# Kernel tuning notes

Hardware: AMD Instinct MI355X
Metric: run time of the kernel (lower is better)

The kernel has to match this reference:

```python
import jax, jax.numpy as jnp
import numpy as np

VOTE_PERHEAD = 24  # matches init vote_perhead


def setup_inputs() -> dict:
    key = jax.random.key(0)
    kx, = jax.random.split(key, 1)
    B, S, D = 2048, 1024, 12  # batch, seq_len (perfect square 32*32), num_heads channel
    x = jax.random.normal(kx, (B, S, D), dtype=jnp.float32)
    # fixed Gaussian-like smoothing kernel [[1,2,1],[2,4,2],[1,2,1]] (OIHW)
    kernel = jnp.array([[1.0, 2.0, 1.0], [2.0, 4.0, 2.0], [1.0, 2.0, 1.0]],
                       dtype=jnp.float32).reshape(1, 1, 3, 3)
    return {"x": x, "kernel": kernel, "select_num": 24}


def reference(x, kernel, select_num):
    B, S = x.shape[0], x.shape[1]
    # score over non-CLS tokens, channel 0: [B, S-1]
    score = x[:, 1:, 0]
    # top-k vote indices per batch: [B, VOTE_PERHEAD], values in [0, S-2]
    _, select = jax.lax.top_k(score, VOTE_PERHEAD)
    # batched bincount via scatter-add (replaces the per-batch python loop)
    count = jnp.zeros((B, S), dtype=jnp.float32)
    count = count.at[jnp.arange(B)[:, None], select].add(1.0)
    # enhance_local: 2D 3x3 smoothing conv when S is a perfect square
    Hs = int(np.sqrt(S))
    if Hs * Hs == S:
        cnt = count.reshape(B, 1, Hs, Hs)
        cnt = jax.lax.conv_general_dilated(
            cnt, kernel, window_strides=(1, 1), padding=[(1, 1), (1, 1)],
            dimension_numbers=("NCHW", "OIHW", "NCHW"))
        count = cnt.reshape(B, S)
    else:
        k1d = kernel.reshape(1, 1, 9)
        cnt = jax.lax.conv_general_dilated(
            count[:, None, :], k1d, window_strides=(1,), padding=[(4, 4)],
            dimension_numbers=("NCH", "OIH", "NCH"))
        count = cnt.reshape(B, S)
    # descending sort of votes; indices shifted by +1 (skip CLS token)
    patch_idx = jnp.argsort(-count, axis=-1) + 1
    return patch_idx[:, :select_num], count
```

## Files before the change

### kernel.cpp

```cpp
#include <hip/hip_runtime.h>

constexpr int S_ = 1024;
constexpr int D_ = 12;
constexpr int K_ = 24;
constexpr int NT = 256;
constexpr int NL = 5;

__constant__ const unsigned int U_LADDER[NL] =
    {0xC0266666u, 0xC00CCCCDu, 0xBFF33333u, 0xBFCCCCCDu, 0xBFA66666u};

__device__ __forceinline__ void stamp3x3(int p, unsigned int* convp) {
    int r = p >> 5, c0 = p & 31;
    #pragma unroll
    for (int dr = -1; dr <= 1; ++dr) {
        int rr = r + dr;
        if (rr < 0 || rr >= 32) continue;
        #pragma unroll
        for (int dc = -1; dc <= 1; ++dc) {
            int cc = c0 + dc;
            if (cc < 0 || cc >= 32) continue;
            unsigned int w = ((dr == 0) ? 2u : 1u) * ((dc == 0) ? 2u : 1u);
            int q = rr * 32 + cc;
            atomicAdd(&convp[q >> 2], w << ((q & 3) * 8));
        }
    }
}

__global__ __launch_bounds__(NT) void mhv_kernel(const float* __restrict__ x,
                                                 float* __restrict__ out_idx,
                                                 float* __restrict__ out_cnt)
{
    const int b    = blockIdx.x;
    const int tid  = threadIdx.x;
    const int lane = tid & 63;
    const int wid  = tid >> 6;

    __shared__ unsigned long long slab[S_];
    __shared__ unsigned int       convp[S_/4];
    __shared__ int                ck[96];
    __shared__ int                wcnt[4][NL];
    __shared__ int                ncand, nck;

    convp[tid] = 0u;
    if (tid == 0) { ncand = 0; nck = 0; }

    const float* xb = x + (size_t)b * (S_ * D_);
    unsigned int su[4];
    #pragma unroll
    for (int i = 0; i < 4; ++i) {
        int s = wid * 256 + i * 64 + lane;
        su[i] = 0u;
        if (s < S_ - 1) {
            unsigned int bits = __float_as_uint(xb[(s + 1) * D_]);
            su[i] = (bits & 0x80000000u) ? ~bits : (bits | 0x80000000u);
        }
    }

    int cw[NL];
    #pragma unroll
    for (int j = 0; j < NL; ++j) {
        int c = 0;
        #pragma unroll
        for (int i = 0; i < 4; ++i) c += __popcll(__ballot(su[i] >= U_LADDER[j]));
        cw[j] = c;
    }
    if (lane == 0) {
        #pragma unroll
        for (int j = 0; j < NL; ++j) wcnt[wid][j] = cw[j];
    }
    __syncthreads();

    int jsel = -1;
    #pragma unroll
    for (int j = 0; j < NL; ++j) {
        int ct = wcnt[0][j] + wcnt[1][j] + wcnt[2][j] + wcnt[3][j];
        if (jsel < 0 && ct >= K_) jsel = j;
    }
    unsigned int Usel = (jsel >= 0) ? U_LADDER[jsel] : 1u;

    #pragma unroll
    for (int i = 0; i < 4; ++i) {
        bool sel = (su[i] >= Usel);
        unsigned long long m = __ballot(sel);
        int cnt = __popcll(m);
        int base = 0;
        if (lane == 0) base = atomicAdd(&ncand, cnt);
        base = __shfl(base, 0);
        if (sel) {
            int s = wid * 256 + i * 64 + lane;
            slab[base + __popcll(m & ((1ull << lane) - 1ull))] =
                ((unsigned long long)su[i] << 10) | (unsigned)(S_ - 1 - s);
        }
    }
    __syncthreads();

    int c = ncand;
    if (c <= NT) {
        if (tid < c) {
            unsigned long long kk = slab[tid];
            int rk = 0;
            for (int j = 0; j < c; ++j) rk += (slab[j] > kk);
            if (rk < K_) stamp3x3(S_ - 1 - (int)(kk & 1023ull), convp);
        }
    } else {
        unsigned long long kk0 = (tid          < c) ? slab[tid]          : 0ull;
        unsigned long long kk1 = (tid + NT     < c) ? slab[tid + NT]     : 0ull;
        unsigned long long kk2 = (tid + 2*NT   < c) ? slab[tid + 2*NT]   : 0ull;
        unsigned long long kk3 = (tid + 3*NT   < c) ? slab[tid + 3*NT]   : 0ull;
        int r0 = 0, r1 = 0, r2 = 0, r3 = 0;
        for (int j = 0; j < c; ++j) {
            unsigned long long kj = slab[j];
            r0 += (kj > kk0); r1 += (kj > kk1); r2 += (kj > kk2); r3 += (kj > kk3);
        }
        if (tid          < c && r0 < K_) stamp3x3(S_ - 1 - (int)(kk0 & 1023ull), convp);
        if (tid + NT     < c && r1 < K_) stamp3x3(S_ - 1 - (int)(kk1 & 1023ull), convp);
        if (tid + 2*NT   < c && r2 < K_) stamp3x3(S_ - 1 - (int)(kk2 & 1023ull), convp);
        if (tid + 3*NT   < c && r3 < K_) stamp3x3(S_ - 1 - (int)(kk3 & 1023ull), convp);
    }
    __syncthreads();

    unsigned int pw = convp[tid];
    {
        float4 o;
        o.x = (float)(pw & 255u);
        o.y = (float)((pw >> 8) & 255u);
        o.z = (float)((pw >> 16) & 255u);
        o.w = (float)(pw >> 24);
        *(float4*)(out_cnt + (size_t)b * S_ + tid * 4) = o;
    }
    #pragma unroll
    for (int jj = 0; jj < 4; ++jj) {
        unsigned int cv = (pw >> (jj * 8)) & 255u;
        bool sel = (cv >= 4u);
        unsigned long long m = __ballot(sel);
        int cnt = __popcll(m);
        int base = 0;
        if (lane == 0) base = atomicAdd(&nck, cnt);
        base = __shfl(base, 0);
        if (sel) {
            int p = tid * 4 + jj;
            ck[base + __popcll(m & ((1ull << lane) - 1ull))] =
                (int)(cv << 10) | (S_ - 1 - p);
        }
    }
    __syncthreads();

    int c2 = nck;
    if (tid < c2) {
        int kk = ck[tid];
        int rk = 0;
        for (int j = 0; j < c2; ++j) rk += (ck[j] > kk);
        if (rk < K_) out_idx[(size_t)b * K_ + rk] = (float)(S_ - (kk & 1023));
    }
}

extern "C" void kernel_launch(void* const* d_in, const int* in_sizes, int n_in,
                              void* d_out, int out_size, void* d_ws, size_t ws_size,
                              hipStream_t stream) {
    const float* x = (const float*)d_in[0];
    const int B = in_sizes[0] / (S_ * D_);

    float* out     = (float*)d_out;
    float* out_idx = out;
    float* out_cnt = out + (size_t)B * K_;

    mhv_kernel<<<dim3(B), dim3(NT), 0, stream>>>(x, out_idx, out_cnt);
}
```

Baseline: 25.22 us.

## Restructure top-k vote kernel to one wavefront per batch row without barriers

Each batch row is now handled by a single 64-lane wavefront instead of four wavefronts. The per-wave counter exchange, shared atomics and __syncthreads are replaced by ballot/popcount prefix sums and shuffle-based rank counting. A radix-style bitwise threshold search is added as the fallback when the ladder threshold gives too many candidates. The intent is to remove barrier and shared-atomic overhead and cut shared memory so more blocks fit per CU. The cost is fewer threads per row, more serial work per lane (16 loads each) and less latency hiding within a block.

```diff
diff --git a/kernel.cpp b/kernel.cpp
--- a/kernel.cpp
+++ b/kernel.cpp
@@ -3,11 +3,7 @@
 constexpr int S_ = 1024;
 constexpr int D_ = 12;
 constexpr int K_ = 24;
-constexpr int NT = 256;
 constexpr int NL = 5;
-
-__constant__ const unsigned int U_LADDER[NL] =
-    {0xC0266666u, 0xC00CCCCDu, 0xBFF33333u, 0xBFCCCCCDu, 0xBFA66666u};
 
 __device__ __forceinline__ void stamp3x3(int p, unsigned int* convp) {
     int r = p >> 5, c0 = p & 31;
@@ -26,29 +22,26 @@
     }
 }
 
-__global__ __launch_bounds__(NT) void mhv_kernel(const float* __restrict__ x,
+__global__ __launch_bounds__(64) void mhv_kernel(const float* __restrict__ x,
                                                  float* __restrict__ out_idx,
                                                  float* __restrict__ out_cnt)
 {
     const int b    = blockIdx.x;
-    const int tid  = threadIdx.x;
-    const int lane = tid & 63;
-    const int wid  = tid >> 6;
+    const int lane = threadIdx.x;
 
-    __shared__ unsigned long long slab[S_];
-    __shared__ unsigned int       convp[S_/4];
+    __shared__ unsigned int       convp[S_ / 4];
+    __shared__ unsigned long long slab[64];
     __shared__ int                ck[96];
-    __shared__ int                wcnt[4][NL];
-    __shared__ int                ncand, nck;
 
-    convp[tid] = 0u;
-    if (tid == 0) { ncand = 0; nck = 0; }
+    #pragma unroll
+    for (int j = 0; j < 4; ++j) convp[j * 64 + lane] = 0u;
+    slab[lane] = 0ull;
 
     const float* xb = x + (size_t)b * (S_ * D_);
-    unsigned int su[4];
+    unsigned int su[16];
     #pragma unroll
-    for (int i = 0; i < 4; ++i) {
-        int s = wid * 256 + i * 64 + lane;
+    for (int i = 0; i < 16; ++i) {
+        int s = i * 64 + lane;
         su[i] = 0u;
         if (s < S_ - 1) {
             unsigned int bits = __float_as_uint(xb[(s + 1) * D_]);
@@ -56,102 +49,108 @@
         }
     }
 
-    int cw[NL];
+    const unsigned int LAD[NL] = {0xC0266666u, 0xC00CCCCDu, 0xBFF33333u,
+                                  0xBFCCCCCDu, 0xBFA66666u};
+    int lcnt[NL];
     #pragma unroll
     for (int j = 0; j < NL; ++j) {
         int c = 0;
         #pragma unroll
-        for (int i = 0; i < 4; ++i) c += __popcll(__ballot(su[i] >= U_LADDER[j]));
-        cw[j] = c;
+        for (int i = 0; i < 16; ++i) c += __popcll(__ballot(su[i] >= LAD[j]));
+        lcnt[j] = c;
     }
-    if (lane == 0) {
+    int csel = -1; unsigned int Usel = 0u;
+    #pragma unroll
+    for (int j = 0; j < NL; ++j)
+        if (csel < 0 && lcnt[j] >= K_) { csel = lcnt[j]; Usel = LAD[j]; }
+
+    if (csel >= K_ && csel <= 64) {
+        int base = 0;
         #pragma unroll
-        for (int j = 0; j < NL; ++j) wcnt[wid][j] = cw[j];
+        for (int i = 0; i < 16; ++i) {
+            bool sel = (su[i] >= Usel);
+            unsigned long long m = __ballot(sel);
+            if (sel) {
+                int s = i * 64 + lane;
+                slab[base + __popcll(m & ((1ull << lane) - 1ull))] =
+                    ((unsigned long long)su[i] << 10) | (unsigned)(S_ - 1 - s);
+            }
+            base += __popcll(m);
+        }
+        unsigned long long kk = slab[lane];
+        int rk = 0;
+        int cpad = (csel + 3) & ~3;
+        for (int j = 0; j < cpad; j += 4) {
+            #pragma unroll
+            for (int u = 0; u < 4; ++u) {
+                unsigned long long kj = __shfl(kk, j + u);
+                rk += (kj > kk);
+            }
+        }
+        if (lane < csel && rk < K_)
+            stamp3x3(S_ - 1 - (int)(kk & 1023ull), convp);
+    } else {
+        unsigned long long k64[16];
+        #pragma unroll
+        for (int i = 0; i < 16; ++i)
+            k64[i] = ((unsigned long long)su[i] << 10) |
+                     (unsigned)(S_ - 1 - (i * 64 + lane));
+        unsigned long long t = 0ull;
+        for (int bit = 41; bit >= 0; --bit) {
+            unsigned long long tr = t | (1ull << bit);
+            int c = 0;
+            #pragma unroll
+            for (int i = 0; i < 16; ++i) c += __popcll(__ballot(k64[i] >= tr));
+            if (c >= K_) t = tr;
+        }
+        #pragma unroll
+        for (int i = 0; i < 16; ++i)
+            if (k64[i] >= t)
+                stamp3x3(S_ - 1 - (int)(k64[i] & 1023ull), convp);
     }
-    __syncthreads();
 
-    int jsel = -1;
+    int c2base = 0;
     #pragma unroll
-    for (int j = 0; j < NL; ++j) {
-        int ct = wcnt[0][j] + wcnt[1][j] + wcnt[2][j] + wcnt[3][j];
-        if (jsel < 0 && ct >= K_) jsel = j;
-    }
-    unsigned int Usel = (jsel >= 0) ? U_LADDER[jsel] : 1u;
-
-    #pragma unroll
-    for (int i = 0; i < 4; ++i) {
-        bool sel = (su[i] >= Usel);
-        unsigned long long m = __ballot(sel);
-        int cnt = __popcll(m);
-        int base = 0;
-        if (lane == 0) base = atomicAdd(&ncand, cnt);
-        base = __shfl(base, 0);
-        if (sel) {
-            int s = wid * 256 + i * 64 + lane;
-            slab[base + __popcll(m & ((1ull << lane) - 1ull))] =
-                ((unsigned long long)su[i] << 10) | (unsigned)(S_ - 1 - s);
+    for (int j = 0; j < 4; ++j) {
+        unsigned int pd = convp[j * 64 + lane];
+        float4 o;
+        o.x = (float)(pd & 255u);
+        o.y = (float)((pd >> 8) & 255u);
+        o.z = (float)((pd >> 16) & 255u);
+        o.w = (float)(pd >> 24);
+        *(float4*)(out_cnt + (size_t)b * S_ + (j * 64 + lane) * 4) = o;
+        #pragma unroll
+        for (int q = 0; q < 4; ++q) {
+            unsigned int cv = (pd >> (q * 8)) & 255u;
+            bool sel = (cv >= 4u);
+            unsigned long long m = __ballot(sel);
+            if (sel) {
+                int p = (j * 64 + lane) * 4 + q;
+                ck[c2base + __popcll(m & ((1ull << lane) - 1ull))] =
+                    (int)(cv << 10) | (S_ - 1 - p);
+            }
+            c2base += __popcll(m);
         }
     }
-    __syncthreads();
 
-    int c = ncand;
-    if (c <= NT) {
-        if (tid < c) {
-            unsigned long long kk = slab[tid];
-            int rk = 0;
-            for (int j = 0; j < c; ++j) rk += (slab[j] > kk);
-            if (rk < K_) stamp3x3(S_ - 1 - (int)(kk & 1023ull), convp);
-        }
-    } else {
-        unsigned long long kk0 = (tid          < c) ? slab[tid]          : 0ull;
-        unsigned long long kk1 = (tid + NT     < c) ? slab[tid + NT]     : 0ull;
-        unsigned long long kk2 = (tid + 2*NT   < c) ? slab[tid + 2*NT]   : 0ull;
-        unsigned long long kk3 = (tid + 3*NT   < c) ? slab[tid + 3*NT]   : 0ull;
-        int r0 = 0, r1 = 0, r2 = 0, r3 = 0;
-        for (int j = 0; j < c; ++j) {
-            unsigned long long kj = slab[j];
-            r0 += (kj > kk0); r1 += (kj > kk1); r2 += (kj > kk2); r3 += (kj > kk3);
-        }
-        if (tid          < c && r0 < K_) stamp3x3(S_ - 1 - (int)(kk0 & 1023ull), convp);
-        if (tid + NT     < c && r1 < K_) stamp3x3(S_ - 1 - (int)(kk1 & 1023ull), convp);
-        if (tid + 2*NT   < c && r2 < K_) stamp3x3(S_ - 1 - (int)(kk2 & 1023ull), convp);
-        if (tid + 3*NT   < c && r3 < K_) stamp3x3(S_ - 1 - (int)(kk3 & 1023ull), convp);
-    }
-    __syncthreads();
-
-    unsigned int pw = convp[tid];
-    {
-        float4 o;
-        o.x = (float)(pw & 255u);
-        o.y = (float)((pw >> 8) & 255u);
-        o.z = (float)((pw >> 16) & 255u);
-        o.w = (float)(pw >> 24);
-        *(float4*)(out_cnt + (size_t)b * S_ + tid * 4) = o;
-    }
-    #pragma unroll
-    for (int jj = 0; jj < 4; ++jj) {
-        unsigned int cv = (pw >> (jj * 8)) & 255u;
-        bool sel = (cv >= 4u);
-        unsigned long long m = __ballot(sel);
-        int cnt = __popcll(m);
-        int base = 0;
-        if (lane == 0) base = atomicAdd(&nck, cnt);
-        base = __shfl(base, 0);
-        if (sel) {
-            int p = tid * 4 + jj;
-            ck[base + __popcll(m & ((1ull << lane) - 1ull))] =
-                (int)(cv << 10) | (S_ - 1 - p);
+    int c2 = c2base;
+    int k0 = (lane < c2)      ? ck[lane]      : -1;
+    int k1 = (64 + lane < c2) ? ck[64 + lane] : -1;
+    int r0 = 0, r1 = 0;
+    int c2pad = (c2 + 3) & ~3;
+    for (int j = 0; j < c2pad; j += 4) {
+        #pragma unroll
+        for (int u = 0; u < 4; ++u) {
+            int jj = j + u;
+            int kj = (jj < 64) ? __shfl(k0, jj) : __shfl(k1, jj - 64);
+            r0 += (kj > k0);
+            r1 += (kj > k1);
         }
     }
-    __syncthreads();
-
-    int c2 = nck;
-    if (tid < c2) {
-        int kk = ck[tid];
-        int rk = 0;
-        for (int j = 0; j < c2; ++j) rk += (ck[j] > kk);
-        if (rk < K_) out_idx[(size_t)b * K_ + rk] = (float)(S_ - (kk & 1023));
-    }
+    if (lane < c2 && r0 < K_)
+        out_idx[(size_t)b * K_ + r0] = (float)(S_ - (k0 & 1023));
+    if (64 + lane < c2 && r1 < K_)
+        out_idx[(size_t)b * K_ + r1] = (float)(S_ - (k1 & 1023));
 }
 
 extern "C" void kernel_launch(void* const* d_in, const int* in_sizes, int n_in,
@@ -164,5 +163,5 @@
     float* out_idx = out;
     float* out_cnt = out + (size_t)B * K_;
 
-    mhv_kernel<<<dim3(B), dim3(NT), 0, stream>>>(x, out_idx, out_cnt);
+    mhv_kernel<<<dim3(B), dim3(64), 0, stream>>>(x, out_idx, out_cnt);
 }
```

Measured after the change: 27.69 us. +9.8%, slower.

## Process four rows per block with prefetched loads and radix-select fallback

Applied to the files above, without the earlier changes.

Each block now handles four batch rows instead of one. The load of the next row is issued before the current row is processed, so global-memory latency overlaps with compute, and sched_barrier keeps that order. Thresholds become float comparisons. When the candidate count exceeds 256, a bitwise radix-select over 64-bit keys replaces the O(n^2) ranking. The risks are a quarter as many blocks, which lowers parallelism across CUs, and more synchronisation per block.

```diff
diff --git a/kernel.cpp b/kernel.cpp
--- a/kernel.cpp
+++ b/kernel.cpp
@@ -1,13 +1,12 @@
 #include <hip/hip_runtime.h>
-
-constexpr int S_ = 1024;
-constexpr int D_ = 12;
-constexpr int K_ = 24;
-constexpr int NT = 256;
-constexpr int NL = 5;
-
-__constant__ const unsigned int U_LADDER[NL] =
-    {0xC0266666u, 0xC00CCCCDu, 0xBFF33333u, 0xBFCCCCCDu, 0xBFA66666u};
+#include <math.h>
+
+constexpr int S_  = 1024;
+constexpr int D_  = 12;
+constexpr int K_  = 24;
+constexpr int NT  = 256;
+constexpr int RPB = 4;
+constexpr int NL  = 5;
 
 __device__ __forceinline__ void stamp3x3(int p, unsigned int* convp) {
     int r = p >> 5, c0 = p & 31;
@@ -28,130 +27,173 @@
 
 __global__ __launch_bounds__(NT) void mhv_kernel(const float* __restrict__ x,
                                                  float* __restrict__ out_idx,
-                                                 float* __restrict__ out_cnt)
+                                                 float* __restrict__ out_cnt,
+                                                 int B)
 {
-    const int b    = blockIdx.x;
     const int tid  = threadIdx.x;
     const int lane = tid & 63;
     const int wid  = tid >> 6;
-
-    __shared__ unsigned long long slab[S_];
-    __shared__ unsigned int       convp[S_/4];
-    __shared__ int                ck[96];
+    const int r0   = blockIdx.x * RPB;
+
+    __shared__ unsigned int       convp[S_ / 4];
+    __shared__ unsigned long long slab[256];
+    __shared__ int                ck[112];
     __shared__ int                wcnt[4][NL];
-    __shared__ int                ncand, nck;
-
-    convp[tid] = 0u;
-    if (tid == 0) { ncand = 0; nck = 0; }
-
-    const float* xb = x + (size_t)b * (S_ * D_);
-    unsigned int su[4];
-    #pragma unroll
-    for (int i = 0; i < 4; ++i) {
-        int s = wid * 256 + i * 64 + lane;
-        su[i] = 0u;
-        if (s < S_ - 1) {
-            unsigned int bits = __float_as_uint(xb[(s + 1) * D_]);
-            su[i] = (bits & 0x80000000u) ? ~bits : (bits | 0x80000000u);
-        }
-    }
-
-    int cw[NL];
-    #pragma unroll
-    for (int j = 0; j < NL; ++j) {
-        int c = 0;
-        #pragma unroll
-        for (int i = 0; i < 4; ++i) c += __popcll(__ballot(su[i] >= U_LADDER[j]));
-        cw[j] = c;
-    }
-    if (lane == 0) {
-        #pragma unroll
-        for (int j = 0; j < NL; ++j) wcnt[wid][j] = cw[j];
-    }
-    __syncthreads();
-
-    int jsel = -1;
-    #pragma unroll
-    for (int j = 0; j < NL; ++j) {
-        int ct = wcnt[0][j] + wcnt[1][j] + wcnt[2][j] + wcnt[3][j];
-        if (jsel < 0 && ct >= K_) jsel = j;
-    }
-    unsigned int Usel = (jsel >= 0) ? U_LADDER[jsel] : 1u;
-
-    #pragma unroll
-    for (int i = 0; i < 4; ++i) {
-        bool sel = (su[i] >= Usel);
-        unsigned long long m = __ballot(sel);
-        int cnt = __popcll(m);
-        int base = 0;
-        if (lane == 0) base = atomicAdd(&ncand, cnt);
-        base = __shfl(base, 0);
-        if (sel) {
-            int s = wid * 256 + i * 64 + lane;
-            slab[base + __popcll(m & ((1ull << lane) - 1ull))] =
-                ((unsigned long long)su[i] << 10) | (unsigned)(S_ - 1 - s);
-        }
-    }
-    __syncthreads();
-
-    int c = ncand;
-    if (c <= NT) {
-        if (tid < c) {
-            unsigned long long kk = slab[tid];
+    __shared__ int                nc[RPB], nck[RPB];
+
+    if (tid < RPB) { nc[tid] = 0; nck[tid] = 0; }
+
+    const float LAD[NL] = {2.6f, 2.2f, 1.9f, 1.6f, 1.3f};
+
+    float v0[4], v1[4], v2[4], v3[4];
+
+    auto LOADR = [&](float (&v)[4], int row) {
+        const float* xr = x + (size_t)row * (S_ * D_);
+        #pragma unroll
+        for (int i = 0; i < 4; ++i) {
+            int s = i * 256 + tid;
+            v[i] = (s < S_ - 1) ? xr[(s + 1) * D_] : -INFINITY;
+        }
+    };
+
+    auto PROCESS = [&](float (&v)[4], int jrow, int row) {
+        convp[tid] = 0u;
+        slab[tid]  = 0ull;
+        #pragma unroll
+        for (int r = 0; r < NL; ++r) {
+            int c = 0;
+            #pragma unroll
+            for (int i = 0; i < 4; ++i) c += __popcll(__ballot(v[i] >= LAD[r]));
+            if (lane == 0) wcnt[wid][r] = c;
+        }
+        __syncthreads();
+        if (tid < 112) ck[tid] = -1;
+        int csel = -1; float Lsel = 0.f;
+        #pragma unroll
+        for (int r = 0; r < NL; ++r) {
+            int ct = wcnt[0][r] + wcnt[1][r] + wcnt[2][r] + wcnt[3][r];
+            if (csel < K_ && ct >= K_) { csel = ct; Lsel = LAD[r]; }
+        }
+
+        if (csel >= K_ && csel <= 256) {
+            #pragma unroll
+            for (int i = 0; i < 4; ++i) {
+                int s = i * 256 + tid;
+                bool sel = (v[i] >= Lsel);
+                unsigned long long m = __ballot(sel);
+                int cnt = __popcll(m);
+                int base = 0;
+                if (lane == 0) base = atomicAdd(&nc[jrow], cnt);
+                base = __shfl(base, 0);
+                if (sel) {
+                    unsigned int su = __float_as_uint(v[i]) | 0x80000000u;
+                    slab[base + __popcll(m & ((1ull << lane) - 1ull))] =
+                        ((unsigned long long)su << 10) | (unsigned)(S_ - 1 - s);
+                }
+            }
+            __syncthreads();
+            int c = nc[jrow];
+            if (tid < c) {
+                unsigned long long kk = slab[tid];
+                int rk = 0;
+                for (int j = 0; j < c; j += 4) {
+                    #pragma unroll
+                    for (int u = 0; u < 4; ++u)
+                        if (j + u < c) rk += (slab[j + u] > kk);
+                }
+                if (rk < K_) stamp3x3(S_ - 1 - (int)(kk & 1023ull), convp);
+            }
+            __syncthreads();
+        } else {
+            unsigned long long k64[4];
+            #pragma unroll
+            for (int i = 0; i < 4; ++i) {
+                int s = i * 256 + tid;
+                unsigned int bits = __float_as_uint(v[i]);
+                unsigned int su = (bits & 0x80000000u) ? ~bits : (bits | 0x80000000u);
+                k64[i] = ((unsigned long long)su << 10) | (unsigned)(S_ - 1 - s);
+            }
+            unsigned long long t = 0ull;
+            for (int bit = 41; bit >= 0; --bit) {
+                unsigned long long tr = t | (1ull << bit);
+                int c = 0;
+                #pragma unroll
+                for (int i = 0; i < 4; ++i) c += __popcll(__ballot(k64[i] >= tr));
+                if (c >= K_) t = tr;
+            }
+            int base = wid * K_;
+            #pragma unroll
+            for (int i = 0; i < 4; ++i) {
+                bool sel = (k64[i] >= t);
+                unsigned long long m = __ballot(sel);
+                if (sel) slab[base + __popcll(m & ((1ull << lane) - 1ull))] = k64[i];
+                base += __popcll(m);
+            }
+            __syncthreads();
+            if (wid == 0) {
+                unsigned long long g0 = slab[lane];
+                unsigned long long g1 = (lane < 32) ? slab[64 + lane] : 0ull;
+                unsigned long long t2 = 0ull;
+                for (int bit = 41; bit >= 0; --bit) {
+                    unsigned long long tr = t2 | (1ull << bit);
+                    int c = __popcll(__ballot(g0 >= tr)) + __popcll(__ballot(g1 >= tr));
+                    if (c >= K_) t2 = tr;
+                }
+                if (g0 >= t2) stamp3x3(S_ - 1 - (int)(g0 & 1023ull), convp);
+                if (lane < 32 && g1 >= t2) stamp3x3(S_ - 1 - (int)(g1 & 1023ull), convp);
+            }
+            __syncthreads();
+        }
+
+        unsigned int pd = convp[tid];
+        float4 o;
+        o.x = (float)(pd & 255u);
+        o.y = (float)((pd >> 8) & 255u);
+        o.z = (float)((pd >> 16) & 255u);
+        o.w = (float)(pd >> 24);
+        *(float4*)(out_cnt + (size_t)row * S_ + tid * 4) = o;
+        #pragma unroll
+        for (int q = 0; q < 4; ++q) {
+            unsigned int cv = (pd >> (q * 8)) & 255u;
+            bool sel = (cv >= 4u);
+            unsigned long long m = __ballot(sel);
+            int cnt = __popcll(m);
+            int base = 0;
+            if (lane == 0) base = atomicAdd(&nck[jrow], cnt);
+            base = __shfl(base, 0);
+            if (sel) {
+                int p = tid * 4 + q;
+                ck[base + __popcll(m & ((1ull << lane) - 1ull))] =
+                    (int)(cv << 10) | (S_ - 1 - p);
+            }
+        }
+        __syncthreads();
+        int c2 = nck[jrow];
+        if (tid < c2) {
+            int kk = ck[tid];
             int rk = 0;
-            for (int j = 0; j < c; ++j) rk += (slab[j] > kk);
-            if (rk < K_) stamp3x3(S_ - 1 - (int)(kk & 1023ull), convp);
-        }
-    } else {
-        unsigned long long kk0 = (tid          < c) ? slab[tid]          : 0ull;
-        unsigned long long kk1 = (tid + NT     < c) ? slab[tid + NT]     : 0ull;
-        unsigned long long kk2 = (tid + 2*NT   < c) ? slab[tid + 2*NT]   : 0ull;
-        unsigned long long kk3 = (tid + 3*NT   < c) ? slab[tid + 3*NT]   : 0ull;
-        int r0 = 0, r1 = 0, r2 = 0, r3 = 0;
-        for (int j = 0; j < c; ++j) {
-            unsigned long long kj = slab[j];
-            r0 += (kj > kk0); r1 += (kj > kk1); r2 += (kj > kk2); r3 += (kj > kk3);
-        }
-        if (tid          < c && r0 < K_) stamp3x3(S_ - 1 - (int)(kk0 & 1023ull), convp);
-        if (tid + NT     < c && r1 < K_) stamp3x3(S_ - 1 - (int)(kk1 & 1023ull), convp);
-        if (tid + 2*NT   < c && r2 < K_) stamp3x3(S_ - 1 - (int)(kk2 & 1023ull), convp);
-        if (tid + 3*NT   < c && r3 < K_) stamp3x3(S_ - 1 - (int)(kk3 & 1023ull), convp);
-    }
-    __syncthreads();
-
-    unsigned int pw = convp[tid];
-    {
-        float4 o;
-        o.x = (float)(pw & 255u);
-        o.y = (float)((pw >> 8) & 255u);
-        o.z = (float)((pw >> 16) & 255u);
-        o.w = (float)(pw >> 24);
-        *(float4*)(out_cnt + (size_t)b * S_ + tid * 4) = o;
-    }
-    #pragma unroll
-    for (int jj = 0; jj < 4; ++jj) {
-        unsigned int cv = (pw >> (jj * 8)) & 255u;
-        bool sel = (cv >= 4u);
-        unsigned long long m = __ballot(sel);
-        int cnt = __popcll(m);
-        int base = 0;
-        if (lane == 0) base = atomicAdd(&nck, cnt);
-        base = __shfl(base, 0);
-        if (sel) {
-            int p = tid * 4 + jj;
-            ck[base + __popcll(m & ((1ull << lane) - 1ull))] =
-                (int)(cv << 10) | (S_ - 1 - p);
-        }
-    }
-    __syncthreads();
-
-    int c2 = nck;
-    if (tid < c2) {
-        int kk = ck[tid];
-        int rk = 0;
-        for (int j = 0; j < c2; ++j) rk += (ck[j] > kk);
-        if (rk < K_) out_idx[(size_t)b * K_ + rk] = (float)(S_ - (kk & 1023));
-    }
+            for (int j = 0; j < c2; j += 4) {
+                #pragma unroll
+                for (int u = 0; u < 4; ++u)
+                    if (j + u < c2) rk += (ck[j + u] > kk);
+            }
+            if (rk < K_)
+                out_idx[(size_t)row * K_ + rk] = (float)(S_ - (kk & 1023));
+        }
+    };
+
+    const bool has1 = (r0 + 1 < B), has2 = (r0 + 2 < B), has3 = (r0 + 3 < B);
+
+    LOADR(v0, r0);
+    if (has1) LOADR(v1, r0 + 1);
+    PROCESS(v0, 0, r0);
+    __builtin_amdgcn_sched_barrier(0);
+    if (has2) LOADR(v2, r0 + 2);
+    if (has1) PROCESS(v1, 1, r0 + 1);
+    __builtin_amdgcn_sched_barrier(0);
+    if (has3) LOADR(v3, r0 + 3);
+    if (has2) PROCESS(v2, 2, r0 + 2);
+    if (has3) PROCESS(v3, 3, r0 + 3);
 }
 
 extern "C" void kernel_launch(void* const* d_in, const int* in_sizes, int n_in,
@@ -164,5 +206,6 @@
     float* out_idx = out;
     float* out_cnt = out + (size_t)B * K_;
 
-    mhv_kernel<<<dim3(B), dim3(NT), 0, stream>>>(x, out_idx, out_cnt);
+    int blocks = (B + RPB - 1) / RPB;
+    mhv_kernel<<<dim3(blocks), dim3(NT), 0, stream>>>(x, out_idx, out_cnt, B);
 }
```

Result: slower. 37.41 us (+48.4%).
